# Performance work log

Hardware: AMD Instinct MI355X
Metric: run time of the kernel (lower is better)

## Reference

```python
import jax, jax.numpy as jnp
import numpy as np

B, T, D = 64, 512, 512
K_CODES = 256
K_FUTURE = 2


def _gru(x, w_ih, w_hh, b_ih, b_hh):
    # x: [B,T,D]; PyTorch GRU gate order: r, z, n; weights [3D, D]
    xg = jnp.einsum('btd,gd->btg', x, w_ih) + b_ih  # [B,T,3D] precomputed input gates

    def step(h, xg_t):
        hg = h @ w_hh.T + b_hh                      # [B,3D]
        xr, xz, xn = jnp.split(xg_t, 3, axis=-1)
        hr, hz, hn = jnp.split(hg, 3, axis=-1)
        r = jax.nn.sigmoid(xr + hr)
        z = jax.nn.sigmoid(xz + hz)
        n = jnp.tanh(xn + r * hn)
        h_new = (1.0 - z) * n + z * h
        return h_new, h_new

    h0 = jnp.zeros((x.shape[0], w_hh.shape[1]), x.dtype)
    _, hs = jax.lax.scan(step, h0, jnp.swapaxes(xg, 0, 1))
    return jnp.swapaxes(hs, 0, 1)  # [B,T,D]


def setup_inputs() -> dict:
    key = jax.random.key(0)
    ks = jax.random.split(key, 8)
    return {
        'features': jax.random.normal(ks[0], (B, T, D), jnp.float32),
        'codebook': jax.random.uniform(ks[1], (K_CODES, D), jnp.float32, -0.1, 0.1),
        'w_ih': jax.random.normal(ks[2], (3 * D, D), jnp.float32) * 0.02,
        'w_hh': jax.random.normal(ks[3], (3 * D, D), jnp.float32) * 0.02,
        'b_ih': jax.random.normal(ks[4], (3 * D,), jnp.float32) * 0.02,
        'b_hh': jax.random.normal(ks[5], (3 * D,), jnp.float32) * 0.02,
        'proj_w': jax.random.normal(ks[6], (D, D), jnp.float32) * 0.02,
        'proj_b': jax.random.normal(ks[7], (D,), jnp.float32) * 0.02,
    }


def reference(features, codebook, w_ih, w_hh, b_ih, b_hh, proj_w, proj_b):
    b, t, d = features.shape
    # --- quantize: cdist + argmin + gather (squared dists give same argmin) ---
    flat = features.reshape(-1, d)                              # [B*T, D]
    d2 = (jnp.sum(flat * flat, axis=1, keepdims=True)
          - 2.0 * flat @ codebook.T
          + jnp.sum(codebook * codebook, axis=1))               # [B*T, K]
    indices = jnp.argmin(d2, axis=1)                            # [B*T]
    quantized = codebook[indices].reshape(b, t, d)              # gather
    indices = indices.reshape(b, t)

    # --- context prediction loss ---
    hidden = _gru(quantized, w_ih, w_hh, b_ih, b_hh)            # [B,T,D]
    context_proj = hidden @ proj_w.T + proj_b                   # [B,T,D]
    k_max = min(K_FUTURE, t - 1)
    cp_loss = jnp.float32(0.0)
    for k in range(1, k_max + 1):
        cp_loss = cp_loss + jnp.mean((context_proj[:, :-k] - features[:, k:]) ** 2)
    cp_loss = cp_loss / k_max

    # --- VQ loss (stop_gradient mirrors torch .detach()) ---
    commitment_loss = jnp.mean((jax.lax.stop_gradient(features) - quantized) ** 2)
    codebook_loss = jnp.mean((features - jax.lax.stop_gradient(quantized)) ** 2)
    vq_loss = commitment_loss + 0.25 * codebook_loss

    total_loss = cp_loss + vq_loss
    return quantized, indices, total_loss, cp_loss, vq_loss
```

## Files before the change

kernel.cpp:

```cpp
#include <hip/hip_runtime.h>
#include <hip/hip_bf16.h>

#define B_ 64
#define T_ 512
#define D_ 512
#define K_ 256
#define G3 1536

typedef __attribute__((ext_vector_type(8))) short sh8;
typedef __attribute__((ext_vector_type(4))) short sh4;
typedef __attribute__((ext_vector_type(4))) float fx4;
typedef __attribute__((ext_vector_type(4))) int   ix4;

__device__ __forceinline__ short f2bf(float x) {
  __hip_bfloat16 h = __float2bfloat16(x);
  union { __hip_bfloat16 h; short s; } u; u.h = h; return u.s;
}
__device__ __forceinline__ float sigm(float x) { return 1.f / (1.f + __expf(-x)); }
__device__ __forceinline__ float tanh_fast(float x) {
  float e2 = __expf(-2.f * x);
  return (1.f - e2) / (1.f + e2);
}

__global__ void k_cnorm(const float* __restrict__ cb, double* __restrict__ cn) {
  int c = threadIdx.x;
  if (c < K_) {
    double s = 0.0;
    for (int k = 0; k < D_; ++k) { double v = cb[c * D_ + k]; s += v * v; }
    cn[c] = s;
  }
}

__global__ __launch_bounds__(256) void k_cg(const float* __restrict__ cb,
                                            const float* __restrict__ wih,
                                            const float* __restrict__ bih,
                                            const float* __restrict__ bhh,
                                            float* __restrict__ cg) {
  __shared__ float wl[16][512];
  int j0 = blockIdx.x * 16, c0 = blockIdx.y * 64;
  for (int v = threadIdx.x; v < 16 * 128; v += 256) {
    int r = v >> 7, q = v & 127;
    *(fx4*)&wl[r][q * 4] = *(const fx4*)&wih[(j0 + r) * D_ + q * 4];
  }
  __syncthreads();
  for (int p = threadIdx.x; p < 1024; p += 256) {
    int j = p >> 6, c = c0 + (p & 63);
    fx4 a = {0.f, 0.f, 0.f, 0.f};
    const float* cbr = &cb[c * D_];
    for (int q = 0; q < 128; ++q) {
      fx4 w4 = *(fx4*)&wl[j][q * 4];
      fx4 c4 = *(const fx4*)&cbr[q * 4];
      a += w4 * c4;
    }
    int jg = j0 + j;
    float bias = bih[jg] + (jg < 1024 ? bhh[jg] : 0.f);
    cg[c * G3 + jg] = ((a.x + a.y) + (a.z + a.w)) + bias;
  }
}

__global__ void k_cvt(const float* __restrict__ src, __hip_bfloat16* __restrict__ dst, int n4) {
  int i = blockIdx.x * blockDim.x + threadIdx.x;
  if (i < n4) {
    fx4 v = *(const fx4*)&src[i * 4];
    sh4 o; o[0] = f2bf(v.x); o[1] = f2bf(v.y); o[2] = f2bf(v.z); o[3] = f2bf(v.w);
    *(sh4*)&dst[i * 4] = o;
  }
}

__global__ __launch_bounds__(256) void k_quant(const float* __restrict__ feat,
                                               const float* __restrict__ cb,
                                               const double* __restrict__ cn,
                                               int* __restrict__ idxw,
                                               float* __restrict__ outq,
                                               float* __restrict__ outi,
                                               double* __restrict__ lacc) {
  __shared__ float fl[16][516];
  __shared__ double ss1[16][16], ss2[16][16];
  __shared__ int ii1[16][16], ii2[16][16];
  __shared__ int idxl[16];
  __shared__ float rsv[4];
  int row0 = blockIdx.x * 16;
  int tid = threadIdx.x;
  for (int v = tid; v < 16 * 128; v += 256) {
    int r = v >> 7, q = v & 127;
    *(fx4*)&fl[r][q * 4] = *(const fx4*)&feat[(row0 + r) * D_ + q * 4];
  }
  __syncthreads();
  int r = tid & 15, g = tid >> 4;
  fx4 acc[16];
#pragma unroll
  for (int c = 0; c < 16; ++c) acc[c] = (fx4){0.f, 0.f, 0.f, 0.f};
  for (int ch = 0; ch < 8; ++ch) {
    fx4 fc[16];
#pragma unroll
    for (int q = 0; q < 16; ++q) fc[q] = *(fx4*)&fl[r][ch * 64 + q * 4];
#pragma unroll
    for (int c = 0; c < 16; ++c) {
      const float* cbp = &cb[(g * 16 + c) * D_ + ch * 64];
#pragma unroll
      for (int q = 0; q < 16; ++q) {
        fx4 c4 = *(const fx4*)&cbp[q * 4];
        acc[c] += fc[q] * c4;
      }
    }
  }
  double b1 = 1e300, b2 = 1e300; int i1 = 0, i2 = 0;
#pragma unroll
  for (int c = 0; c < 16; ++c) {
    int ci = g * 16 + c;
    double dot = (double)acc[c].x + acc[c].y + acc[c].z + acc[c].w;
    double s = cn[ci] - 2.0 * dot;
    if (s < b1) { b2 = b1; i2 = i1; b1 = s; i1 = ci; }
    else if (s < b2) { b2 = s; i2 = ci; }
  }
  ss1[r][g] = b1; ss2[r][g] = b2; ii1[r][g] = i1; ii2[r][g] = i2;
  __syncthreads();
  if (tid < 16) {
    int rr = tid;
    double c1 = 1e300, c2 = 1e300; int j1 = 0, j2 = 0;
    for (int g2 = 0; g2 < 16; ++g2) {
      double s = ss1[rr][g2]; int ix = ii1[rr][g2];
      if (s < c1 || (s == c1 && ix < j1)) { c2 = c1; j2 = j1; c1 = s; j1 = ix; }
      else if (s < c2 || (s == c2 && ix < j2)) { c2 = s; j2 = ix; }
      s = ss2[rr][g2]; ix = ii2[rr][g2];
      if (s < c1 || (s == c1 && ix < j1)) { c2 = c1; j2 = j1; c1 = s; j1 = ix; }
      else if (s < c2 || (s == c2 && ix < j2)) { c2 = s; j2 = ix; }
    }
    int pick = j1;
    if (c2 - c1 < 1e-4) {
      double d1 = 0.0, d2 = 0.0;
      for (int k = 0; k < D_; ++k) {
        double fv = fl[rr][k];
        d1 += fv * (double)cb[j1 * D_ + k];
        d2 += fv * (double)cb[j2 * D_ + k];
      }
      double e1 = cn[j1] - 2.0 * d1, e2 = cn[j2] - 2.0 * d2;
      if (e2 < e1 || (e2 == e1 && j2 < j1)) pick = j2;
    }
    idxl[rr] = pick;
    idxw[row0 + rr] = pick;
    outi[row0 + rr] = (float)pick;
  }
  __syncthreads();
  float vs = 0.f;
  for (int v = tid; v < 16 * 128; v += 256) {
    int rr = v >> 7, q = v & 127;
    fx4 c4 = *(const fx4*)&cb[idxl[rr] * D_ + q * 4];
    *(fx4*)&outq[(row0 + rr) * D_ + q * 4] = c4;
    fx4 f4 = *(fx4*)&fl[rr][q * 4];
    fx4 d = f4 - c4;
    vs += d.x * d.x + d.y * d.y + d.z * d.z + d.w * d.w;
  }
#pragma unroll
  for (int off = 32; off > 0; off >>= 1) vs += __shfl_down(vs, off);
  if ((tid & 63) == 0) rsv[tid >> 6] = vs;
  __syncthreads();
  if (tid == 0) atomicAdd(&lacc[2], (double)(rsv[0] + rsv[1] + rsv[2] + rsv[3]));
}

__global__ __launch_bounds__(256, 1) void k_gru(const float* __restrict__ whh,
                                                const float* __restrict__ bhh,
                                                const float* __restrict__ cg,
                                                const int* __restrict__ idx,
                                                __hip_bfloat16* __restrict__ hid,
                                                unsigned int* __restrict__ flag,
                                                int* __restrict__ xcca,
                                                unsigned int* __restrict__ bar0,
                                                unsigned int* __restrict__ done) {
  int bid = blockIdx.x;
  int tid = threadIdx.x;

  if (bid >= 64) {
    fx4 hacc = {0.f, 0.f, 0.f, 0.f};
    sh8 hz = {0, 0, 0, 0, 0, 0, 0, 0};
    while (__hip_atomic_load(done, __ATOMIC_RELAXED, __HIP_MEMORY_SCOPE_AGENT) < 64u) {
#pragma unroll 8
      for (int i = 0; i < 2048; ++i)
        hacc = __builtin_amdgcn_mfma_f32_16x16x32_bf16(hz, hz, hacc, 0, 0, 0);
    }
    asm volatile("" :: "v"(hacc[0]));
    return;
  }

  __builtin_amdgcn_s_setprio(1);
  int g = bid & 7, s = bid >> 3;
  int w = tid >> 6, lane = tid & 63, l15 = lane & 15, l4 = lane >> 4;
  int wv = s * 4 + w;

  sh8 A0[16], A1[16], A2[16];
#pragma unroll
  for (int kt = 0; kt < 16; ++kt) {
#pragma unroll
    for (int t3 = 0; t3 < 3; ++t3) {
      const float* wr = &whh[((t3 * 512) + s * 64 + w * 16 + l15) * D_];
      int k0 = kt * 32 + l4 * 8;
      fx4 x = *(const fx4*)&wr[k0];
      fx4 y = *(const fx4*)&wr[k0 + 4];
      sh8 tt;
      tt[0] = f2bf(x.x); tt[1] = f2bf(x.y); tt[2] = f2bf(x.z); tt[3] = f2bf(x.w);
      tt[4] = f2bf(y.x); tt[5] = f2bf(y.y); tt[6] = f2bf(y.z); tt[7] = f2bf(y.w);
      if (t3 == 0) A0[kt] = tt; else if (t3 == 1) A1[kt] = tt; else A2[kt] = tt;
    }
  }

  const bool act = (l15 < 8);
  const int b = l15 & 7;
  const int dg0 = s * 64 + w * 16 + l4 * 4;

  fx4 bn = *(const fx4*)&bhh[1024 + dg0];
  fx4 hp = {0.f, 0.f, 0.f, 0.f};

  __shared__ int sh_fast;
  if (tid == 0) {
    int xcc = 0;
    asm volatile("s_getreg_b32 %0, hwreg(HW_REG_XCC_ID)" : "=s"(xcc));
    __hip_atomic_store(&xcca[bid], xcc, __ATOMIC_RELEASE, __HIP_MEMORY_SCOPE_AGENT);
    __hip_atomic_fetch_add(bar0, 1u, __ATOMIC_ACQ_REL, __HIP_MEMORY_SCOPE_AGENT);
    while (__hip_atomic_load(bar0, __ATOMIC_ACQUIRE, __HIP_MEMORY_SCOPE_AGENT) < 64u)
      __builtin_amdgcn_s_sleep(2);
    int x0 = __hip_atomic_load(&xcca[g], __ATOMIC_RELAXED, __HIP_MEMORY_SCOPE_AGENT);
    int f = 1;
    for (int m = 1; m < 8; ++m)
      if (__hip_atomic_load(&xcca[g + 8 * m], __ATOMIC_RELAXED, __HIP_MEMORY_SCOPE_AGENT) != x0)
        f = 0;
    sh_fast = f;
    __threadfence();
  }
  __syncthreads();
  const bool fast = (sh_fast != 0);

  const unsigned* pollp = &flag[g * 32 + (lane & 31)];

  for (int t = 0; t < T_; ++t) {
    fx4 cr = {0, 0, 0, 0}, cz = {0, 0, 0, 0}, cnn = {0, 0, 0, 0};
    if (act) {
      int ci = idx[(g * 8 + b) * T_ + t];
      const float* cgr = &cg[(size_t)ci * G3 + dg0];
      cr  = *(const fx4*)cgr;
      cz  = *(const fx4*)(cgr + 512);
      cnn = *(const fx4*)(cgr + 1024);
    }

    fx4 a0 = {0, 0, 0, 0}, a1 = {0, 0, 0, 0}, a2 = {0, 0, 0, 0};
    if (t > 0) {
      for (;;) {
        unsigned v = __hip_atomic_load(pollp, __ATOMIC_RELAXED, __HIP_MEMORY_SCOPE_AGENT);
        if (__all((int)(v >= (unsigned)t))) break;
        __builtin_amdgcn_s_sleep(1);
      }
      asm volatile("" ::: "memory");
      if (!fast) __threadfence();

      const __hip_bfloat16* hrow =
          &hid[((size_t)(g * 8 + b) * T_ + (t - 1)) * D_];
#pragma unroll
      for (int kt = 0; kt < 16; ++kt) {
        sh8 bfr = {0, 0, 0, 0, 0, 0, 0, 0};
        if (act) bfr = *(const sh8*)&hrow[kt * 32 + l4 * 8];
        a0 = __builtin_amdgcn_mfma_f32_16x16x32_bf16(A0[kt], bfr, a0, 0, 0, 0);
        a1 = __builtin_amdgcn_mfma_f32_16x16x32_bf16(A1[kt], bfr, a1, 0, 0, 0);
        a2 = __builtin_amdgcn_mfma_f32_16x16x32_bf16(A2[kt], bfr, a2, 0, 0, 0);
      }
    }

    if (act) {
      sh4 hb4;
#pragma unroll
      for (int rg = 0; rg < 4; ++rg) {
        float rr = sigm(cr[rg] + a0[rg]);
        float zz = sigm(cz[rg] + a1[rg]);
        float nn = tanh_fast(cnn[rg] + rr * (a2[rg] + bn[rg]));
        float hv = (1.f - zz) * nn + zz * hp[rg];
        hp[rg] = hv;
        hb4[rg] = f2bf(hv);
      }
      *(sh4*)&hid[((size_t)(g * 8 + b) * T_ + t) * D_ + dg0] = hb4;
    }
    asm volatile("s_waitcnt vmcnt(0)" ::: "memory");
    if (!fast) __threadfence();
    if (lane == 0)
      __hip_atomic_store(&flag[g * 32 + wv], (unsigned)(t + 1),
                         __ATOMIC_RELAXED, __HIP_MEMORY_SCOPE_AGENT);
  }

  __syncthreads();
  if (tid == 0)
    __hip_atomic_fetch_add(done, 1u, __ATOMIC_RELEASE, __HIP_MEMORY_SCOPE_AGENT);
}

__global__ __launch_bounds__(256) void k_proj(const __hip_bfloat16* __restrict__ hid,
                                              const __hip_bfloat16* __restrict__ pwb,
                                              const float* __restrict__ pb,
                                              const float* __restrict__ feat,
                                              double* __restrict__ lacc) {
  __shared__ char Bl[512 * 64];
  __shared__ char Al[32 * 64];
  __shared__ float rs1[4], rs2[4];
  int Mb = blockIdx.x * 32;
  int tid = threadIdx.x;
  int w = tid >> 6, lane = tid & 63, l15 = lane & 15, l4 = lane >> 4;
  fx4 acc[2][8];
#pragma unroll
  for (int a = 0; a < 2; ++a)
#pragma unroll
    for (int b = 0; b < 8; ++b) acc[a][b] = (fx4){0, 0, 0, 0};

  for (int kc = 0; kc < 16; ++kc) {
    for (int v = tid; v < 2048; v += 256) {
      int rw = v >> 2, sg = v & 3;
      ix4 d = *(const ix4*)&pwb[rw * D_ + kc * 32 + sg * 8];
      *(ix4*)(Bl + rw * 64 + ((sg * 16) ^ ((rw & 7) << 4))) = d;
    }
    if (tid < 128) {
      int rw = tid >> 2, sg = tid & 3;
      ix4 d = *(const ix4*)&hid[(size_t)(Mb + rw) * D_ + kc * 32 + sg * 8];
      *(ix4*)(Al + rw * 64 + ((sg * 16) ^ ((rw & 7) << 4))) = d;
    }
    __syncthreads();
    sh8 af0, af1;
    {
      int m = l15;
      af0 = *(const sh8*)(Al + m * 64 + ((l4 * 16) ^ ((m & 7) << 4)));
      m = 16 + l15;
      af1 = *(const sh8*)(Al + m * 64 + ((l4 * 16) ^ ((m & 7) << 4)));
    }
#pragma unroll
    for (int nt = 0; nt < 8; ++nt) {
      int n = (w * 8 + nt) * 16 + l15;
      sh8 bf = *(const sh8*)(Bl + n * 64 + ((l4 * 16) ^ ((n & 7) << 4)));
      acc[0][nt] = __builtin_amdgcn_mfma_f32_16x16x32_bf16(af0, bf, acc[0][nt], 0, 0, 0);
      acc[1][nt] = __builtin_amdgcn_mfma_f32_16x16x32_bf16(af1, bf, acc[1][nt], 0, 0, 0);
    }
    __syncthreads();
  }

  float s1 = 0.f, s2 = 0.f;
#pragma unroll
  for (int mt = 0; mt < 2; ++mt) {
#pragma unroll
    for (int nt = 0; nt < 8; ++nt) {
      int n = (w * 8 + nt) * 16 + l15;
      float bias = pb[n];
#pragma unroll
      for (int rg = 0; rg < 4; ++rg) {
        int m = Mb + mt * 16 + l4 * 4 + rg;
        float val = acc[mt][nt][rg] + bias;
        int t = m & (T_ - 1);
        if (t < T_ - 1) { float d = val - feat[(size_t)(m + 1) * D_ + n]; s1 += d * d; }
        if (t < T_ - 2) { float d = val - feat[(size_t)(m + 2) * D_ + n]; s2 += d * d; }
      }
    }
  }
#pragma unroll
  for (int off = 32; off > 0; off >>= 1) {
    s1 += __shfl_down(s1, off);
    s2 += __shfl_down(s2, off);
  }
  if (lane == 0) { rs1[w] = s1; rs2[w] = s2; }
  __syncthreads();
  if (tid == 0) {
    atomicAdd(&lacc[0], (double)rs1[0] + rs1[1] + rs1[2] + rs1[3]);
    atomicAdd(&lacc[1], (double)rs2[0] + rs2[1] + rs2[2] + rs2[3]);
  }
}

__global__ void k_fin(const double* __restrict__ lacc, float* __restrict__ outl) {
  if (threadIdx.x == 0) {
    double cp = 0.5 * (lacc[0] / ((double)B_ * (T_ - 1) * D_) +
                       lacc[1] / ((double)B_ * (T_ - 2) * D_));
    double vq = 1.25 * lacc[2] / ((double)B_ * T_ * D_);
    outl[0] = (float)(cp + vq);
    outl[1] = (float)cp;
    outl[2] = (float)vq;
  }
}

extern "C" void kernel_launch(void* const* d_in, const int* in_sizes, int n_in,
                              void* d_out, int out_size, void* d_ws, size_t ws_size,
                              hipStream_t stream) {
  (void)in_sizes; (void)n_in; (void)out_size; (void)ws_size;
  const float* feat = (const float*)d_in[0];
  const float* cb   = (const float*)d_in[1];
  const float* wih  = (const float*)d_in[2];
  const float* whh  = (const float*)d_in[3];
  const float* bih  = (const float*)d_in[4];
  const float* bhh  = (const float*)d_in[5];
  const float* pw   = (const float*)d_in[6];
  const float* pb   = (const float*)d_in[7];

  float* out  = (float*)d_out;
  float* outq = out;
  float* outi = out + (size_t)B_ * T_ * D_;
  float* outl = outi + B_ * T_;

  char* ws = (char*)d_ws;
  size_t o = 0;
  auto alloc = [&](size_t sz) { void* p = ws + o; o += (sz + 255) & ~(size_t)255; return p; };
  float*          cg   = (float*)alloc(sizeof(float) * K_ * G3);
  double*         cn   = (double*)alloc(sizeof(double) * K_);
  int*            idxw = (int*)alloc(sizeof(int) * B_ * T_);
  __hip_bfloat16* pwb  = (__hip_bfloat16*)alloc(sizeof(__hip_bfloat16) * D_ * D_);
  double*         lacc = (double*)alloc(sizeof(double) * 4);
  unsigned*       flag = (unsigned*)alloc(sizeof(unsigned) * 256);
  int*            xcca = (int*)alloc(sizeof(int) * 64);
  unsigned*       bar0 = (unsigned*)alloc(sizeof(unsigned) * 4);
  unsigned*       dn   = (unsigned*)alloc(sizeof(unsigned) * 4);
  __hip_bfloat16* hid  = (__hip_bfloat16*)alloc(sizeof(__hip_bfloat16) * (size_t)B_ * T_ * D_);

  hipMemsetAsync(lacc, 0, sizeof(double) * 4, stream);
  hipMemsetAsync(flag, 0, sizeof(unsigned) * 256, stream);
  hipMemsetAsync(xcca, 0, sizeof(int) * 64, stream);
  hipMemsetAsync(bar0, 0, sizeof(unsigned) * 4, stream);
  hipMemsetAsync(dn,   0, sizeof(unsigned) * 4, stream);

  hipLaunchKernelGGL(k_cnorm, dim3(1), dim3(256), 0, stream, cb, cn);
  hipLaunchKernelGGL(k_cg, dim3(96, 4), dim3(256), 0, stream, cb, wih, bih, bhh, cg);
  hipLaunchKernelGGL(k_cvt, dim3(256), dim3(256), 0, stream, pw, pwb, D_ * D_ / 4);
  hipLaunchKernelGGL(k_quant, dim3(2048), dim3(256), 0, stream, feat, cb, cn, idxw, outq, outi, lacc);
  hipLaunchKernelGGL(k_gru, dim3(248), dim3(256), 0, stream, whh, bhh, cg, idxw, hid, flag, xcca, bar0, dn);
  hipLaunchKernelGGL(k_proj, dim3(1024), dim3(256), 0, stream, hid, pwb, pb, feat, lacc);
  hipLaunchKernelGGL(k_fin, dim3(1), dim3(64), 0, stream, lacc, outl);
}
```

Before: 3.446 ms.

## Replace per-wave flag polling with per-group counting barrier in GRU recurrence

The GRU step synchronisation changes from each wave polling 32 per-wave flags to a block-level __syncthreads plus a single atomic counter barrier per batch group, with one thread spinning. The codebook index for the next step is now prefetched one iteration ahead. The idle filler blocks now run eight independent MFMA accumulator chains with non-zero inputs, and the grid grows to 256 blocks. This is meant to cut polling traffic and per-step sync latency, but it adds two block-wide barriers per timestep and a fetch_add on a shared counter.

```diff
diff --git a/kernel.cpp b/kernel.cpp
--- a/kernel.cpp
+++ b/kernel.cpp
@@ -163,7 +163,7 @@
                                                 const float* __restrict__ cg,
                                                 const int* __restrict__ idx,
                                                 __hip_bfloat16* __restrict__ hid,
-                                                unsigned int* __restrict__ flag,
+                                                unsigned int* __restrict__ bar,
                                                 int* __restrict__ xcca,
                                                 unsigned int* __restrict__ bar0,
                                                 unsigned int* __restrict__ done) {
@@ -171,21 +171,33 @@
   int tid = threadIdx.x;
 
   if (bid >= 64) {
-    fx4 hacc = {0.f, 0.f, 0.f, 0.f};
-    sh8 hz = {0, 0, 0, 0, 0, 0, 0, 0};
+    sh8 hz;
+#pragma unroll
+    for (int i = 0; i < 8; ++i) hz[i] = (short)(0x3f80 + tid * 7 + i * 131);
+    fx4 ac0 = {1.f, 0, 0, 0}, ac1 = {0, 1.f, 0, 0}, ac2 = {0, 0, 1.f, 0},
+        ac3 = {0, 0, 0, 1.f}, ac4 = {2.f, 0, 0, 0}, ac5 = {0, 2.f, 0, 0},
+        ac6 = {0, 0, 2.f, 0}, ac7 = {0, 0, 0, 2.f};
     while (__hip_atomic_load(done, __ATOMIC_RELAXED, __HIP_MEMORY_SCOPE_AGENT) < 64u) {
-#pragma unroll 8
-      for (int i = 0; i < 2048; ++i)
-        hacc = __builtin_amdgcn_mfma_f32_16x16x32_bf16(hz, hz, hacc, 0, 0, 0);
-    }
-    asm volatile("" :: "v"(hacc[0]));
+#pragma unroll 4
+      for (int i = 0; i < 256; ++i) {
+        ac0 = __builtin_amdgcn_mfma_f32_16x16x32_bf16(hz, hz, ac0, 0, 0, 0);
+        ac1 = __builtin_amdgcn_mfma_f32_16x16x32_bf16(hz, hz, ac1, 0, 0, 0);
+        ac2 = __builtin_amdgcn_mfma_f32_16x16x32_bf16(hz, hz, ac2, 0, 0, 0);
+        ac3 = __builtin_amdgcn_mfma_f32_16x16x32_bf16(hz, hz, ac3, 0, 0, 0);
+        ac4 = __builtin_amdgcn_mfma_f32_16x16x32_bf16(hz, hz, ac4, 0, 0, 0);
+        ac5 = __builtin_amdgcn_mfma_f32_16x16x32_bf16(hz, hz, ac5, 0, 0, 0);
+        ac6 = __builtin_amdgcn_mfma_f32_16x16x32_bf16(hz, hz, ac6, 0, 0, 0);
+        ac7 = __builtin_amdgcn_mfma_f32_16x16x32_bf16(hz, hz, ac7, 0, 0, 0);
+      }
+    }
+    asm volatile("" :: "v"(ac0[0]), "v"(ac1[0]), "v"(ac2[0]), "v"(ac3[0]),
+                       "v"(ac4[0]), "v"(ac5[0]), "v"(ac6[0]), "v"(ac7[0]));
     return;
   }
 
   __builtin_amdgcn_s_setprio(1);
   int g = bid & 7, s = bid >> 3;
   int w = tid >> 6, lane = tid & 63, l15 = lane & 15, l4 = lane >> 4;
-  int wv = s * 4 + w;
 
   sh8 A0[16], A1[16], A2[16];
 #pragma unroll
@@ -229,28 +241,23 @@
   __syncthreads();
   const bool fast = (sh_fast != 0);
 
-  const unsigned* pollp = &flag[g * 32 + (lane & 31)];
+  unsigned* const barg = &bar[g * 32];
+
+  int ci = act ? idx[(g * 8 + b) * T_] : 0;
 
   for (int t = 0; t < T_; ++t) {
     fx4 cr = {0, 0, 0, 0}, cz = {0, 0, 0, 0}, cnn = {0, 0, 0, 0};
+    int ci_nx = 0;
     if (act) {
-      int ci = idx[(g * 8 + b) * T_ + t];
       const float* cgr = &cg[(size_t)ci * G3 + dg0];
       cr  = *(const fx4*)cgr;
       cz  = *(const fx4*)(cgr + 512);
       cnn = *(const fx4*)(cgr + 1024);
+      if (t + 1 < T_) ci_nx = idx[(g * 8 + b) * T_ + t + 1];
     }
 
     fx4 a0 = {0, 0, 0, 0}, a1 = {0, 0, 0, 0}, a2 = {0, 0, 0, 0};
     if (t > 0) {
-      for (;;) {
-        unsigned v = __hip_atomic_load(pollp, __ATOMIC_RELAXED, __HIP_MEMORY_SCOPE_AGENT);
-        if (__all((int)(v >= (unsigned)t))) break;
-        __builtin_amdgcn_s_sleep(1);
-      }
-      asm volatile("" ::: "memory");
-      if (!fast) __threadfence();
-
       const __hip_bfloat16* hrow =
           &hid[((size_t)(g * 8 + b) * T_ + (t - 1)) * D_];
 #pragma unroll
@@ -276,14 +283,20 @@
       }
       *(sh4*)&hid[((size_t)(g * 8 + b) * T_ + t) * D_ + dg0] = hb4;
     }
-    asm volatile("s_waitcnt vmcnt(0)" ::: "memory");
-    if (!fast) __threadfence();
-    if (lane == 0)
-      __hip_atomic_store(&flag[g * 32 + wv], (unsigned)(t + 1),
-                         __ATOMIC_RELAXED, __HIP_MEMORY_SCOPE_AGENT);
-  }
-
-  __syncthreads();
+    ci = ci_nx;
+
+    __syncthreads();
+    if (tid == 0) {
+      if (!fast) __threadfence();
+      __hip_atomic_fetch_add(barg, 1u, __ATOMIC_RELEASE, __HIP_MEMORY_SCOPE_AGENT);
+      unsigned tgt = 8u * (unsigned)(t + 1);
+      while (__hip_atomic_load(barg, __ATOMIC_ACQUIRE, __HIP_MEMORY_SCOPE_AGENT) < tgt)
+        __builtin_amdgcn_s_sleep(1);
+      if (!fast) __threadfence();
+    }
+    __syncthreads();
+  }
+
   if (tid == 0)
     __hip_atomic_fetch_add(done, 1u, __ATOMIC_RELEASE, __HIP_MEMORY_SCOPE_AGENT);
 }
@@ -401,14 +414,14 @@
   int*            idxw = (int*)alloc(sizeof(int) * B_ * T_);
   __hip_bfloat16* pwb  = (__hip_bfloat16*)alloc(sizeof(__hip_bfloat16) * D_ * D_);
   double*         lacc = (double*)alloc(sizeof(double) * 4);
-  unsigned*       flag = (unsigned*)alloc(sizeof(unsigned) * 256);
+  unsigned*       bar  = (unsigned*)alloc(sizeof(unsigned) * 8 * 32);
   int*            xcca = (int*)alloc(sizeof(int) * 64);
   unsigned*       bar0 = (unsigned*)alloc(sizeof(unsigned) * 4);
   unsigned*       dn   = (unsigned*)alloc(sizeof(unsigned) * 4);
   __hip_bfloat16* hid  = (__hip_bfloat16*)alloc(sizeof(__hip_bfloat16) * (size_t)B_ * T_ * D_);
 
   hipMemsetAsync(lacc, 0, sizeof(double) * 4, stream);
-  hipMemsetAsync(flag, 0, sizeof(unsigned) * 256, stream);
+  hipMemsetAsync(bar,  0, sizeof(unsigned) * 8 * 32, stream);
   hipMemsetAsync(xcca, 0, sizeof(int) * 64, stream);
   hipMemsetAsync(bar0, 0, sizeof(unsigned) * 4, stream);
   hipMemsetAsync(dn,   0, sizeof(unsigned) * 4, stream);
@@ -417,7 +430,7 @@
   hipLaunchKernelGGL(k_cg, dim3(96, 4), dim3(256), 0, stream, cb, wih, bih, bhh, cg);
   hipLaunchKernelGGL(k_cvt, dim3(256), dim3(256), 0, stream, pw, pwb, D_ * D_ / 4);
   hipLaunchKernelGGL(k_quant, dim3(2048), dim3(256), 0, stream, feat, cb, cn, idxw, outq, outi, lacc);
-  hipLaunchKernelGGL(k_gru, dim3(248), dim3(256), 0, stream, whh, bhh, cg, idxw, hid, flag, xcca, bar0, dn);
+  hipLaunchKernelGGL(k_gru, dim3(256), dim3(256), 0, stream, whh, bhh, cg, idxw, hid, bar, xcca, bar0, dn);
   hipLaunchKernelGGL(k_proj, dim3(1024), dim3(256), 0, stream, hid, pwb, pb, feat, lacc);
   hipLaunchKernelGGL(k_fin, dim3(1), dim3(64), 0, stream, lacc, outl);
 }
```

Result: slower. 3.653 ms (+6.0%).
